# Kernel tuning notes

Measured on AMD Instinct MI355X. Metric: run time of the kernel, lower is better.

Reference implementation:

```python
import jax, jax.numpy as jnp
import numpy as np

B, TAU, T0V, D, PD, RD, DO, K = 2048, 32, 96, 64, 3, 1, 64, 16
R = 1.0  # radius for radius_graph


def setup_inputs() -> dict:
    key = jax.random.key(0)
    ks = jax.random.split(key, 9)
    return {
        "x": jax.random.normal(ks[0], (B, TAU, D), jnp.float32),
        "pos": jax.random.uniform(ks[1], (B, TAU, PD), jnp.float32),
        "rot": jax.random.uniform(ks[2], (B, TAU, RD), jnp.float32),
        "old_x": jax.random.normal(ks[3], (B, 128, D), jnp.float32),
        "old_pos": jax.random.uniform(ks[4], (B, 128, PD), jnp.float32),
        "old_rot": jax.random.uniform(ks[5], (B, 128, RD), jnp.float32),
        "W_self": jax.random.normal(ks[6], (D + PD + RD, DO), jnp.float32) * 0.1,
        "W_nbr": jax.random.normal(ks[7], (D + PD + RD, DO), jnp.float32) * 0.1,
        "bias": jax.random.normal(ks[8], (DO,), jnp.float32) * 0.1,
        "T0": T0V,
        "tau": TAU,
    }


def reference(x, pos, rot, old_x, old_pos, old_rot, W_self, W_nbr, bias, T0, tau):
    # --- update(): scatter new observations into the state buffers ---
    # (regular case: T[b]=T0, taus[b]=tau for all b, so new_idx is a static slice)
    new_x = old_x.at[:, T0:T0 + tau].set(x)
    new_pos = old_pos.at[:, T0:T0 + tau].set(pos)
    new_rot = old_rot.at[:, T0:T0 + tau].set(rot)

    L = T0 + tau  # valid (non-padded) nodes per env
    nx, npv, nr = new_x[:, :L], new_pos[:, :L], new_rot[:, :L]
    h = jnp.concatenate([nx, npv, nr], axis=-1)  # [B, L, D+PD+RD] node features

    # --- radius_graph(r, max_num_neighbors=K, loop=True) + remove_noncausal_edges ---
    # edge (j -> i) kept iff ||pos_j - pos_i|| <= r and j < i (causal, drops self-loops)
    diff = npv[:, :, None, :] - npv[:, None, :, :]           # [B, L, L, PD]
    d2 = jnp.sum(diff * diff, axis=-1)                        # [B, L, L] (target i, source j)
    t_idx = jnp.arange(L)
    causal = t_idx[None, :] < t_idx[:, None]                  # [L, L] j < i
    mask = causal[None, :, :] & (d2 <= R * R)
    masked_d2 = jnp.where(mask, d2, jnp.inf)
    neg_d, nbr_idx = jax.lax.top_k(-masked_d2, K)             # k nearest causal in-radius
    valid = jnp.isfinite(neg_d)                               # [B, L, K]

    # --- gnn(): one message-passing layer (stand-in for external gnn) ---
    msg = h @ W_nbr                                           # [B, L, DO]
    gathered = jax.vmap(lambda m, i: m[i])(msg, nbr_idx)      # [B, L, K, DO]
    agg = jnp.sum(gathered * valid[..., None].astype(msg.dtype), axis=2)
    out = jax.nn.relu(h @ W_self + agg + bias)                # [B, L, DO]

    # --- gather flat_new_idx / scatter into padded output ---
    padded_output = out[:, T0:T0 + tau]                       # [B, tau, DO]
    return padded_output, new_x, new_pos, new_rot
```

## Files before the change

### kernel.cpp

```cpp
#include <hip/hip_runtime.h>
#include <hip/hip_bf16.h>
#include <cstdint>
#include <cstddef>

#define NB 2048
#define TAU 32
#define T0C 96
#define LQ 128
#define DD 64
#define DOUT 64
#define KK 16
#define INVK 0xFFFFFFFFu

typedef unsigned int u32;
typedef __attribute__((ext_vector_type(8))) short short8;
typedef __attribute__((ext_vector_type(4))) float f32x4;

__device__ __forceinline__ float fmul_exact(float a, float b) {
  float r; asm("v_mul_f32 %0, %1, %2" : "=v"(r) : "v"(a), "v"(b)); return r;
}
__device__ __forceinline__ float fadd_exact(float a, float b) {
  float r; asm("v_add_f32 %0, %1, %2" : "=v"(r) : "v"(a), "v"(b)); return r;
}
__device__ __forceinline__ unsigned short f2bf(float f) {
  __hip_bfloat16 h = __float2bfloat16(f);
  return *reinterpret_cast<unsigned short*>(&h);
}
__device__ __forceinline__ u32 shfl_xor_u32(u32 v, int mask) {
  return (u32)__shfl_xor((int)v, mask, 64);
}

__device__ __forceinline__ void barrier_lgkm() {
  asm volatile("s_waitcnt lgkmcnt(0)" ::: "memory");
  __builtin_amdgcn_s_barrier();
  __builtin_amdgcn_sched_barrier(0);
}

#define CA(i, j) { u32 _lo = min(kd[i], kd[j]); u32 _hi = max(kd[i], kd[j]); kd[i] = _lo; kd[j] = _hi; }
#define CD(i, j) { u32 _lo = min(kd[i], kd[j]); u32 _hi = max(kd[i], kd[j]); kd[i] = _hi; kd[j] = _lo; }

#define SORT16() do { \
  CA(0,1)  CD(2,3)  CA(4,5)  CD(6,7)  CA(8,9)  CD(10,11) CA(12,13) CD(14,15) \
  CA(0,2)  CA(1,3)  CD(4,6)  CD(5,7)  CA(8,10) CA(9,11)  CD(12,14) CD(13,15) \
  CA(0,1)  CA(2,3)  CD(4,5)  CD(6,7)  CA(8,9)  CA(10,11) CD(12,13) CD(14,15) \
  CA(0,4)  CA(1,5)  CA(2,6)  CA(3,7)  CD(8,12) CD(9,13)  CD(10,14) CD(11,15) \
  CA(0,2)  CA(1,3)  CA(4,6)  CA(5,7)  CD(8,10) CD(9,11)  CD(12,14) CD(13,15) \
  CA(0,1)  CA(2,3)  CA(4,5)  CA(6,7)  CD(8,9)  CD(10,11) CD(12,13) CD(14,15) \
  CA(0,8)  CA(1,9)  CA(2,10) CA(3,11) CA(4,12) CA(5,13)  CA(6,14)  CA(7,15)  \
  CA(0,4)  CA(1,5)  CA(2,6)  CA(3,7)  CA(8,12) CA(9,13)  CA(10,14) CA(11,15) \
  CA(0,2)  CA(1,3)  CA(4,6)  CA(5,7)  CA(8,10) CA(9,11)  CA(12,14) CA(13,15) \
  CA(0,1)  CA(2,3)  CA(4,5)  CA(6,7)  CA(8,9)  CA(10,11) CA(12,13) CA(14,15) \
} while (0)

#define MERGE16() do { \
  CA(0,8)  CA(1,9)  CA(2,10) CA(3,11) CA(4,12) CA(5,13)  CA(6,14)  CA(7,15)  \
  CA(0,4)  CA(1,5)  CA(2,6)  CA(3,7)  CA(8,12) CA(9,13)  CA(10,14) CA(11,15) \
  CA(0,2)  CA(1,3)  CA(4,6)  CA(5,7)  CA(8,10) CA(9,11)  CA(12,14) CA(13,15) \
  CA(0,1)  CA(2,3)  CA(4,5)  CA(6,7)  CA(8,9)  CA(10,11) CA(12,13) CA(14,15) \
} while (0)

#define SHUF_MERGE(mask) do { \
  u32 pb[16]; \
  _Pragma("unroll") \
  for (int _i = 0; _i < 16; ++_i) pb[_i] = shfl_xor_u32(kd[15 - _i], mask); \
  _Pragma("unroll") \
  for (int _i = 0; _i < 16; ++_i) kd[_i] = min(kd[_i], pb[_i]); \
  MERGE16(); \
} while (0)

__global__ __launch_bounds__(256) void prep_w(
    const float* __restrict__ W_nbr, const float* __restrict__ W_self,
    unsigned short* __restrict__ wst) {
  int idx = blockIdx.x * 256 + threadIdx.x;
  int m = idx & 4095;
  int n = m >> 6, k = m & 63;
  const float* src = (idx < 4096) ? W_nbr : W_self;
  wst[idx] = f2bf(src[k * DOUT + n]);
}

__global__ __launch_bounds__(256, 4) void navgcm_fused(
    const float* __restrict__ x, const float* __restrict__ pos_in, const float* __restrict__ rot_in,
    const float* __restrict__ old_x, const float* __restrict__ old_pos, const float* __restrict__ old_rot,
    const float* __restrict__ W_self, const float* __restrict__ W_nbr, const float* __restrict__ bias,
    const unsigned short* __restrict__ wst,
    float* __restrict__ outp)
{
  const int b = blockIdx.x;
  const int tid = threadIdx.x;
  const int lane = tid & 63;
  const int wv = tid >> 6;
  const int fr = lane & 15;
  const int fg = lane >> 4;

  __shared__ __align__(16) unsigned short HsT[64 * 136];
  __shared__ __align__(16) unsigned short Hq[32 * 72];
  __shared__ __align__(16) unsigned short Pm[32][136];
  __shared__ float px[LQ], py[LQ], pz[LQ], rt[LQ];

  const bool haspos = tid < LQ;
  float p0 = 0.f, p1 = 0.f, p2 = 0.f, rr = 0.f;
  if (haspos) {
    int t = tid;
    if (t < T0C) {
      const float* s = old_pos + ((size_t)b * LQ + t) * 3;
      p0 = s[0]; p1 = s[1]; p2 = s[2];
      rr = old_rot[(size_t)b * LQ + t];
    } else {
      const float* s = pos_in + ((size_t)b * TAU + (t - T0C)) * 3;
      p0 = s[0]; p1 = s[1]; p2 = s[2];
      rr = rot_in[(size_t)b * TAU + (t - T0C)];
    }
  }

  float4 v[8];
  #pragma unroll
  for (int it = 0; it < 8; ++it) {
    int n = tid + 256 * it;
    int row = n >> 4, c4 = n & 15;
    const float4* src = (row < T0C)
        ? (const float4*)(old_x + ((size_t)b * LQ + row) * DD)
        : (const float4*)(x + ((size_t)b * TAU + (row - T0C)) * DD);
    v[it] = src[c4];
  }

  {
    u32* pz32 = (u32*)&Pm[0][0];
    #pragma unroll
    for (int k = 0; k < 9; ++k) {
      int idx = tid + 256 * k;
      if (idx < 2176) pz32[idx] = 0u;
    }
  }

  float* dpos = outp + (size_t)NB * TAU * DOUT + (size_t)NB * LQ * DD;
  float* drot = dpos + (size_t)NB * LQ * 3;
  if (haspos) {
    px[tid] = p0; py[tid] = p1; pz[tid] = p2; rt[tid] = rr;
    size_t g = (size_t)b * LQ + tid;
    dpos[g * 3 + 0] = p0; dpos[g * 3 + 1] = p1; dpos[g * 3 + 2] = p2;
    drot[g] = rr;
  }
  barrier_lgkm();

  {
    const int q = tid >> 3, s8 = tid & 7;
    const int i = T0C + q;
    const float pix = px[i], piy = py[i], piz = pz[i];

    u32 kb[16];
    #pragma unroll
    for (int c = 0; c < 16; ++c) {
      int j = 8 * c + s8;
      float dx = pix - px[j], dy = piy - py[j], dz = piz - pz[j];
      float d2 = fadd_exact(fadd_exact(fmul_exact(dx, dx), fmul_exact(dy, dy)),
                            fmul_exact(dz, dz));
      bool valid = (d2 <= 1.0f) && (j < i);
      kb[c] = valid ? __float_as_uint(d2) : INVK;
    }

    u32 kd[16];
    #pragma unroll
    for (int c = 0; c < 16; ++c) kd[c] = kb[c];
    SORT16();
    SHUF_MERGE(1);
    SHUF_MERGE(2);
    SHUF_MERGE(4);

    const u32 T = kd[15];
    int nless = 0;
    #pragma unroll
    for (int t = 0; t < KK; ++t) nless += (kd[t] < T) ? 1 : 0;
    const int needT = (T == INVK) ? 0 : (KK - nless);

    u32 selmask = 0;
    #pragma unroll
    for (int c = 0; c < 16; ++c) selmask |= (kb[c] < T) ? (1u << c) : 0u;

    u32 em = 0;
    #pragma unroll
    for (int c = 0; c < 16; ++c) em |= (kb[c] == T) ? (1u << c) : 0u;
    if (T == INVK) em = 0;
    for (int t = 0; __any(t < needT); ++t) {
      bool act = t < needT;
      u32 myj = (act && em) ? (u32)(8 * __builtin_ctz(em) + s8) : 0xFFFFu;
      u32 gj = myj;
      gj = min(gj, shfl_xor_u32(gj, 1));
      gj = min(gj, shfl_xor_u32(gj, 2));
      gj = min(gj, shfl_xor_u32(gj, 4));
      if (act && myj == gj && myj != 0xFFFFu) {
        int c = __builtin_ctz(em);
        selmask |= 1u << c;
        em &= em - 1;
      }
    }

    u32 m = selmask;
    while (m) {
      int c = __builtin_ctz(m);
      m &= m - 1;
      Pm[q][8 * c + s8] = 0x3F80;
    }

    float g0 = 0.f, g1 = 0.f, g2 = 0.f, g3 = 0.f;
    u32 m2 = selmask;
    while (m2) {
      int c = __builtin_ctz(m2);
      m2 &= m2 - 1;
      int j = 8 * c + s8;
      g0 += px[j]; g1 += py[j]; g2 += pz[j]; g3 += rt[j];
    }
    g0 += __shfl_xor(g0, 1, 64); g0 += __shfl_xor(g0, 2, 64); g0 += __shfl_xor(g0, 4, 64);
    g1 += __shfl_xor(g1, 1, 64); g1 += __shfl_xor(g1, 2, 64); g1 += __shfl_xor(g1, 4, 64);
    g2 += __shfl_xor(g2, 1, 64); g2 += __shfl_xor(g2, 2, 64); g2 += __shfl_xor(g2, 4, 64);
    g3 += __shfl_xor(g3, 1, 64); g3 += __shfl_xor(g3, 2, 64); g3 += __shfl_xor(g3, 4, 64);
    if (s8 == 0) {
      float4 gv; gv.x = g0; gv.y = g1; gv.z = g2; gv.w = g3;
      *reinterpret_cast<float4*>(&Pm[q][128]) = gv;
    }
  }

  float4* dnx = (float4*)(outp + (size_t)NB * TAU * DOUT);
  #pragma unroll
  for (int it = 0; it < 8; ++it) {
    int n = tid + 256 * it;
    int row = n >> 4, c4 = n & 15;
    unsigned short w0 = f2bf(v[it].x), w1 = f2bf(v[it].y),
                   w2 = f2bf(v[it].z), w3 = f2bf(v[it].w);
    int rj = row ^ ((c4 & 7) << 3);
    HsT[(4 * c4 + 0) * 136 + rj] = w0;
    HsT[(4 * c4 + 1) * 136 + rj] = w1;
    HsT[(4 * c4 + 2) * 136 + rj] = w2;
    HsT[(4 * c4 + 3) * 136 + rj] = w3;
    if (it >= 6) {
      ushort4 w4; w4.x = w0; w4.y = w1; w4.z = w2; w4.w = w3;
      *reinterpret_cast<ushort4*>(&Hq[(row - T0C) * 72 + c4 * 4]) = w4;
    }
    dnx[(size_t)b * 2048 + n] = v[it];
  }
  barrier_lgkm();

  const unsigned short* wn_t = wst;
  const unsigned short* ws_t = wst + 4096;
  const int mt = wv & 1;
  const int ntb = (wv >> 1) * 2;

  f32x4 accG[2];
  #pragma unroll
  for (int n = 0; n < 2; ++n) accG[n] = (f32x4){0.f, 0.f, 0.f, 0.f};
  #pragma unroll
  for (int ks = 0; ks < 4; ++ks) {
    short8 pa = *reinterpret_cast<const short8*>(&Pm[mt * 16 + fr][ks * 32 + fg * 8]);
    #pragma unroll
    for (int ntl = 0; ntl < 2; ++ntl) {
      int nf = (ntb + ntl) * 16 + fr;
      int j0 = (ks * 32 + fg * 8) ^ (((nf >> 2) & 7) << 3);
      short8 hb = *reinterpret_cast<const short8*>(&HsT[nf * 136 + j0]);
      accG[ntl] = __builtin_amdgcn_mfma_f32_16x16x32_bf16(pa, hb, accG[ntl], 0, 0, 0);
    }
  }

  short8 aQ0 = *reinterpret_cast<const short8*>(&Hq[(mt * 16 + fr) * 72 + fg * 8]);
  short8 aQ1 = *reinterpret_cast<const short8*>(&Hq[(mt * 16 + fr) * 72 + 32 + fg * 8]);
  f32x4 acc2[2];
  #pragma unroll
  for (int n = 0; n < 2; ++n) acc2[n] = (f32x4){0.f, 0.f, 0.f, 0.f};
  #pragma unroll
  for (int ntl = 0; ntl < 2; ++ntl) {
    int nt = ntb + ntl;
    short8 b0 = *reinterpret_cast<const short8*>(&ws_t[(nt * 16 + fr) * 64 + fg * 8]);
    short8 b1 = *reinterpret_cast<const short8*>(&ws_t[(nt * 16 + fr) * 64 + 32 + fg * 8]);
    acc2[ntl] = __builtin_amdgcn_mfma_f32_16x16x32_bf16(aQ0, b0, acc2[ntl], 0, 0, 0);
    acc2[ntl] = __builtin_amdgcn_mfma_f32_16x16x32_bf16(aQ1, b1, acc2[ntl], 0, 0, 0);
  }
  barrier_lgkm();

  #pragma unroll
  for (int ntl = 0; ntl < 2; ++ntl) {
    int nf = (ntb + ntl) * 16 + fr;
    #pragma unroll
    for (int r = 0; r < 4; ++r) {
      int q = mt * 16 + fg * 4 + r;
      Hq[q * 72 + nf] = f2bf(accG[ntl][r]);
    }
  }
  barrier_lgkm();

  f32x4 agg4[2];
  #pragma unroll
  for (int n = 0; n < 2; ++n) agg4[n] = (f32x4){0.f, 0.f, 0.f, 0.f};
  #pragma unroll
  for (int ks = 0; ks < 2; ++ks) {
    short8 ga = *reinterpret_cast<const short8*>(&Hq[(mt * 16 + fr) * 72 + ks * 32 + fg * 8]);
    #pragma unroll
    for (int ntl = 0; ntl < 2; ++ntl) {
      short8 wb = *reinterpret_cast<const short8*>(&wn_t[((ntb + ntl) * 16 + fr) * 64 + ks * 32 + fg * 8]);
      agg4[ntl] = __builtin_amdgcn_mfma_f32_16x16x32_bf16(ga, wb, agg4[ntl], 0, 0, 0);
    }
  }

  float4 gpv[4];
  #pragma unroll
  for (int r = 0; r < 4; ++r)
    gpv[r] = *reinterpret_cast<const float4*>(&Pm[mt * 16 + fg * 4 + r][128]);

  #pragma unroll
  for (int ntl = 0; ntl < 2; ++ntl) {
    int col = (ntb + ntl) * 16 + fr;
    float wn0 = W_nbr[64 * DOUT + col], wn1 = W_nbr[65 * DOUT + col];
    float wn2 = W_nbr[66 * DOUT + col], wn3 = W_nbr[67 * DOUT + col];
    float ws0 = W_self[64 * DOUT + col], ws1 = W_self[65 * DOUT + col];
    float ws2 = W_self[66 * DOUT + col], ws3 = W_self[67 * DOUT + col];
    float bi = bias[col];
    #pragma unroll
    for (int r = 0; r < 4; ++r) {
      int q = mt * 16 + fg * 4 + r;
      int row = T0C + q;
      float vv = acc2[ntl][r] + agg4[ntl][r] + bi
               + gpv[r].x * wn0 + gpv[r].y * wn1 + gpv[r].z * wn2 + gpv[r].w * wn3
               + px[row] * ws0 + py[row] * ws1 + pz[row] * ws2 + rt[row] * ws3;
      vv = fmaxf(vv, 0.f);
      outp[((size_t)b * TAU + q) * DOUT + col] = vv;
    }
  }
}

extern "C" void kernel_launch(void* const* d_in, const int* in_sizes, int n_in,
                              void* d_out, int out_size, void* d_ws, size_t ws_size,
                              hipStream_t stream) {
  (void)in_sizes; (void)n_in; (void)ws_size; (void)out_size;
  const float* x       = (const float*)d_in[0];
  const float* pos     = (const float*)d_in[1];
  const float* rot     = (const float*)d_in[2];
  const float* old_x   = (const float*)d_in[3];
  const float* old_pos = (const float*)d_in[4];
  const float* old_rot = (const float*)d_in[5];
  const float* W_self  = (const float*)d_in[6];
  const float* W_nbr   = (const float*)d_in[7];
  const float* bias    = (const float*)d_in[8];
  float* out = (float*)d_out;
  unsigned short* wst = (unsigned short*)d_ws;

  hipLaunchKernelGGL(prep_w, dim3(32), dim3(256), 0, stream, W_nbr, W_self, wst);
  hipLaunchKernelGGL(navgcm_fused, dim3(NB), dim3(256), 0, stream,
                     x, pos, rot, old_x, old_pos, old_rot, W_self, W_nbr, bias, wst, out);
}
```

Baseline: 39.52 us.

## Prefetch weight fragments early, use nontemporal stores, and raise priority around MFMAs

Bf16 weight fragments for both MFMA stages are now loaded from global memory into registers before the first barrier, and the fp32 tail weights and bias are loaded before a later barrier, so their latency overlaps other work instead of sitting in the matmul path. All output stores (copied state buffers, positions, rotations, final output) become nontemporal to reduce cache pollution. s_setprio is raised around the MFMA sections. The early loads add register pressure under launch_bounds(256,4), which could cause spills or lower occupancy.

```diff
diff --git a/kernel.cpp b/kernel.cpp
--- a/kernel.cpp
+++ b/kernel.cpp
@@ -91,6 +91,8 @@
   const int wv = tid >> 6;
   const int fr = lane & 15;
   const int fg = lane >> 4;
+  const int mt = wv & 1;
+  const int ntb = (wv >> 1) * 2;
 
   __shared__ __align__(16) unsigned short HsT[64 * 136];
   __shared__ __align__(16) unsigned short Hq[32 * 72];
@@ -112,14 +114,14 @@
     }
   }
 
-  float4 v[8];
+  f32x4 v[8];
   #pragma unroll
   for (int it = 0; it < 8; ++it) {
     int n = tid + 256 * it;
     int row = n >> 4, c4 = n & 15;
-    const float4* src = (row < T0C)
-        ? (const float4*)(old_x + ((size_t)b * LQ + row) * DD)
-        : (const float4*)(x + ((size_t)b * TAU + (row - T0C)) * DD);
+    const f32x4* src = (row < T0C)
+        ? (const f32x4*)(old_x + ((size_t)b * LQ + row) * DD)
+        : (const f32x4*)(x + ((size_t)b * TAU + (row - T0C)) * DD);
     v[it] = src[c4];
   }
 
@@ -127,8 +129,8 @@
     u32* pz32 = (u32*)&Pm[0][0];
     #pragma unroll
     for (int k = 0; k < 9; ++k) {
-      int idx = tid + 256 * k;
-      if (idx < 2176) pz32[idx] = 0u;
+      int idx2 = tid + 256 * k;
+      if (idx2 < 2176) pz32[idx2] = 0u;
     }
   }
 
@@ -137,8 +139,10 @@
   if (haspos) {
     px[tid] = p0; py[tid] = p1; pz[tid] = p2; rt[tid] = rr;
     size_t g = (size_t)b * LQ + tid;
-    dpos[g * 3 + 0] = p0; dpos[g * 3 + 1] = p1; dpos[g * 3 + 2] = p2;
-    drot[g] = rr;
+    __builtin_nontemporal_store(p0, &dpos[g * 3 + 0]);
+    __builtin_nontemporal_store(p1, &dpos[g * 3 + 1]);
+    __builtin_nontemporal_store(p2, &dpos[g * 3 + 2]);
+    __builtin_nontemporal_store(rr, &drot[g]);
   }
   barrier_lgkm();
 
@@ -214,12 +218,24 @@
     g2 += __shfl_xor(g2, 1, 64); g2 += __shfl_xor(g2, 2, 64); g2 += __shfl_xor(g2, 4, 64);
     g3 += __shfl_xor(g3, 1, 64); g3 += __shfl_xor(g3, 2, 64); g3 += __shfl_xor(g3, 4, 64);
     if (s8 == 0) {
-      float4 gv; gv.x = g0; gv.y = g1; gv.z = g2; gv.w = g3;
-      *reinterpret_cast<float4*>(&Pm[q][128]) = gv;
-    }
-  }
-
-  float4* dnx = (float4*)(outp + (size_t)NB * TAU * DOUT);
+      f32x4 gv = (f32x4){g0, g1, g2, g3};
+      *reinterpret_cast<f32x4*>(&Pm[q][128]) = gv;
+    }
+  }
+
+  const unsigned short* wn_t = wst;
+  const unsigned short* ws_t = wst + 4096;
+  short8 bS[2][2], wbE[2][2];
+  #pragma unroll
+  for (int ntl = 0; ntl < 2; ++ntl) {
+    int nt = ntb + ntl;
+    bS[ntl][0] = *reinterpret_cast<const short8*>(&ws_t[(nt * 16 + fr) * 64 + fg * 8]);
+    bS[ntl][1] = *reinterpret_cast<const short8*>(&ws_t[(nt * 16 + fr) * 64 + 32 + fg * 8]);
+    wbE[ntl][0] = *reinterpret_cast<const short8*>(&wn_t[(nt * 16 + fr) * 64 + fg * 8]);
+    wbE[ntl][1] = *reinterpret_cast<const short8*>(&wn_t[(nt * 16 + fr) * 64 + 32 + fg * 8]);
+  }
+
+  f32x4* dnx = (f32x4*)(outp + (size_t)NB * TAU * DOUT);
   #pragma unroll
   for (int it = 0; it < 8; ++it) {
     int n = tid + 256 * it;
@@ -235,18 +251,14 @@
       ushort4 w4; w4.x = w0; w4.y = w1; w4.z = w2; w4.w = w3;
       *reinterpret_cast<ushort4*>(&Hq[(row - T0C) * 72 + c4 * 4]) = w4;
     }
-    dnx[(size_t)b * 2048 + n] = v[it];
+    __builtin_nontemporal_store(v[it], &dnx[(size_t)b * 2048 + n]);
   }
   barrier_lgkm();
 
-  const unsigned short* wn_t = wst;
-  const unsigned short* ws_t = wst + 4096;
-  const int mt = wv & 1;
-  const int ntb = (wv >> 1) * 2;
-
   f32x4 accG[2];
   #pragma unroll
   for (int n = 0; n < 2; ++n) accG[n] = (f32x4){0.f, 0.f, 0.f, 0.f};
+  __builtin_amdgcn_s_setprio(1);
   #pragma unroll
   for (int ks = 0; ks < 4; ++ks) {
     short8 pa = *reinterpret_cast<const short8*>(&Pm[mt * 16 + fr][ks * 32 + fg * 8]);
@@ -266,12 +278,10 @@
   for (int n = 0; n < 2; ++n) acc2[n] = (f32x4){0.f, 0.f, 0.f, 0.f};
   #pragma unroll
   for (int ntl = 0; ntl < 2; ++ntl) {
-    int nt = ntb + ntl;
-    short8 b0 = *reinterpret_cast<const short8*>(&ws_t[(nt * 16 + fr) * 64 + fg * 8]);
-    short8 b1 = *reinterpret_cast<const short8*>(&ws_t[(nt * 16 + fr) * 64 + 32 + fg * 8]);
-    acc2[ntl] = __builtin_amdgcn_mfma_f32_16x16x32_bf16(aQ0, b0, acc2[ntl], 0, 0, 0);
-    acc2[ntl] = __builtin_amdgcn_mfma_f32_16x16x32_bf16(aQ1, b1, acc2[ntl], 0, 0, 0);
-  }
+    acc2[ntl] = __builtin_amdgcn_mfma_f32_16x16x32_bf16(aQ0, bS[ntl][0], acc2[ntl], 0, 0, 0);
+    acc2[ntl] = __builtin_amdgcn_mfma_f32_16x16x32_bf16(aQ1, bS[ntl][1], acc2[ntl], 0, 0, 0);
+  }
+  __builtin_amdgcn_s_setprio(0);
   barrier_lgkm();
 
   #pragma unroll
@@ -283,43 +293,52 @@
       Hq[q * 72 + nf] = f2bf(accG[ntl][r]);
     }
   }
+
+  float wn4[2][4], ws4[2][4], bi2[2];
+  #pragma unroll
+  for (int ntl = 0; ntl < 2; ++ntl) {
+    int col = (ntb + ntl) * 16 + fr;
+    wn4[ntl][0] = W_nbr[64 * DOUT + col]; wn4[ntl][1] = W_nbr[65 * DOUT + col];
+    wn4[ntl][2] = W_nbr[66 * DOUT + col]; wn4[ntl][3] = W_nbr[67 * DOUT + col];
+    ws4[ntl][0] = W_self[64 * DOUT + col]; ws4[ntl][1] = W_self[65 * DOUT + col];
+    ws4[ntl][2] = W_self[66 * DOUT + col]; ws4[ntl][3] = W_self[67 * DOUT + col];
+    bi2[ntl] = bias[col];
+  }
   barrier_lgkm();
 
   f32x4 agg4[2];
   #pragma unroll
   for (int n = 0; n < 2; ++n) agg4[n] = (f32x4){0.f, 0.f, 0.f, 0.f};
+  __builtin_amdgcn_s_setprio(1);
   #pragma unroll
   for (int ks = 0; ks < 2; ++ks) {
     short8 ga = *reinterpret_cast<const short8*>(&Hq[(mt * 16 + fr) * 72 + ks * 32 + fg * 8]);
     #pragma unroll
     for (int ntl = 0; ntl < 2; ++ntl) {
-      short8 wb = *reinterpret_cast<const short8*>(&wn_t[((ntb + ntl) * 16 + fr) * 64 + ks * 32 + fg * 8]);
-      agg4[ntl] = __builtin_amdgcn_mfma_f32_16x16x32_bf16(ga, wb, agg4[ntl], 0, 0, 0);
-    }
-  }
-
-  float4 gpv[4];
+      agg4[ntl] = __builtin_amdgcn_mfma_f32_16x16x32_bf16(ga, wbE[ntl][ks], agg4[ntl], 0, 0, 0);
+    }
+  }
+  __builtin_amdgcn_s_setprio(0);
+
+  f32x4 gpv[4];
   #pragma unroll
   for (int r = 0; r < 4; ++r)
-    gpv[r] = *reinterpret_cast<const float4*>(&Pm[mt * 16 + fg * 4 + r][128]);
+    gpv[r] = *reinterpret_cast<const f32x4*>(&Pm[mt * 16 + fg * 4 + r][128]);
 
   #pragma unroll
   for (int ntl = 0; ntl < 2; ++ntl) {
     int col = (ntb + ntl) * 16 + fr;
-    float wn0 = W_nbr[64 * DOUT + col], wn1 = W_nbr[65 * DOUT + col];
-    float wn2 = W_nbr[66 * DOUT + col], wn3 = W_nbr[67 * DOUT + col];
-    float ws0 = W_self[64 * DOUT + col], ws1 = W_self[65 * DOUT + col];
-    float ws2 = W_self[66 * DOUT + col], ws3 = W_self[67 * DOUT + col];
-    float bi = bias[col];
     #pragma unroll
     for (int r = 0; r < 4; ++r) {
       int q = mt * 16 + fg * 4 + r;
       int row = T0C + q;
-      float vv = acc2[ntl][r] + agg4[ntl][r] + bi
-               + gpv[r].x * wn0 + gpv[r].y * wn1 + gpv[r].z * wn2 + gpv[r].w * wn3
-               + px[row] * ws0 + py[row] * ws1 + pz[row] * ws2 + rt[row] * ws3;
+      float vv = acc2[ntl][r] + agg4[ntl][r] + bi2[ntl]
+               + gpv[r].x * wn4[ntl][0] + gpv[r].y * wn4[ntl][1]
+               + gpv[r].z * wn4[ntl][2] + gpv[r].w * wn4[ntl][3]
+               + px[row] * ws4[ntl][0] + py[row] * ws4[ntl][1]
+               + pz[row] * ws4[ntl][2] + rt[row] * ws4[ntl][3];
       vv = fmaxf(vv, 0.f);
-      outp[((size_t)b * TAU + q) * DOUT + col] = vv;
+      __builtin_nontemporal_store(vv, &outp[((size_t)b * TAU + q) * DOUT + col]);
     }
   }
 }
```

Measured after the change: 38.01 us (median of 3 runs). 3.8% less time.
